# Kernel optimization log

Measured on AMD Instinct MI355X. Metric: run time of the kernel, lower is better.

## Reference

```python
import jax, jax.numpy as jnp
import numpy as np

EPS = 1e-5
NUM_CRYSTALS = 64


def _bn(x2d, g, b):
    # torch BatchNorm1d in training mode: biased batch stats, affine
    m = x2d.mean(0)
    v = x2d.var(0)
    return g * (x2d - m) * jax.lax.rsqrt(v + EPS) + b


def _improved_conv(x, e, idx, p):
    (fcW, fcb, g1, b1, g2, b2, eW, eb, ge, be, W3, b3, g3, b3b) = p
    N, M = idx.shape
    A = x.shape[1]
    Bf = e.shape[2]
    xn = x[idx]  # (N, M, A) gathered neighbor atom features
    tot = jnp.concatenate([jnp.broadcast_to(x[:, None, :], (N, M, A)), xn, e], axis=2)  # (N,M,2A+B)
    # 2-body gated message
    h = jnp.einsum('nmf,of->nmo', tot, fcW) + fcb
    h = _bn(h.reshape(-1, 2 * A), g1, b1).reshape(N, M, 2 * A)
    two_body = jnp.sum(jax.nn.sigmoid(h[..., :A]) * jax.nn.softplus(h[..., A:]), axis=1)
    # explicit edge update
    he = jnp.einsum('nmf,of->nmo', tot, eW) + eb
    he = _bn(he.reshape(-1, 2 * Bf), ge, be).reshape(N, M, 2 * Bf)
    e_out = e + jax.nn.sigmoid(he[..., :Bf]) * jax.nn.softplus(he[..., Bf:])
    # 3-body: split W3 by concat blocks [x_i, x_j, x_l, e_ij, e_il] so the
    # (N,M,M,3A+2B) concat is never materialized; only (N,M,M,2A) is formed.
    Wa, Wj, Wl, Wij, Wil = jnp.split(W3, [A, 2 * A, 3 * A, 3 * A + Bf], axis=1)
    h3 = ((x @ Wa.T)[:, None, None, :]
          + (xn @ Wj.T)[:, :, None, :]
          + (xn @ Wl.T)[:, None, :, :]
          + (e @ Wij.T)[:, :, None, :]
          + (e @ Wil.T)[:, None, :, :]
          + b3)  # (N, M, M, 2A)
    h3 = _bn(h3.reshape(-1, 2 * A), g3, b3b).reshape(N, M, M, 2 * A)
    three_body = jnp.sum(jax.nn.sigmoid(h3[..., :A]) * jax.nn.softplus(h3[..., A:]), axis=(1, 2))
    total = _bn(two_body + three_body, g2, b2)
    return jax.nn.softplus(x + total), e_out


def setup_inputs() -> dict:
    key = jax.random.key(0)
    ks = jax.random.split(key, 12)
    N, M, OF, A, BF, H, NC = 2000, 12, 92, 64, 41, 128, 3
    f = lambda k, s: jax.random.normal(k, s, dtype=jnp.float32) * 0.05
    z = lambda s: jnp.zeros(s, jnp.float32)
    o = lambda s: jnp.ones(s, jnp.float32)
    return {
        'atom_fea': jax.random.normal(ks[0], (N, OF), dtype=jnp.float32),
        'nbr_fea': jax.random.normal(ks[1], (N, M, BF), dtype=jnp.float32),
        'nbr_fea_idx': jax.random.randint(ks[2], (N, M), 0, N),
        'site_seg': jnp.sort(jax.random.randint(ks[3], (N,), 0, NUM_CRYSTALS)),
        'emb_W': f(ks[4], (A, OF)), 'emb_b': z((A,)),
        'fcW': f(ks[5], (NC, 2 * A, 2 * A + BF)), 'fcb': z((NC, 2 * A)),
        'bn1_g': o((NC, 2 * A)), 'bn1_b': z((NC, 2 * A)),
        'bn2_g': o((NC, A)), 'bn2_b': z((NC, A)),
        'eW': f(ks[6], (NC, 2 * BF, 2 * A + BF)), 'eb': z((NC, 2 * BF)),
        'bne_g': o((NC, 2 * BF)), 'bne_b': z((NC, 2 * BF)),
        'W3': f(ks[7], (NC, 2 * A, 3 * A + 2 * BF)), 'b3': z((NC, 2 * A)),
        'bn3_g': o((NC, 2 * A)), 'bn3_b': z((NC, 2 * A)),
        'fc1W': f(ks[8], (H, A)), 'fc1b': z((H,)),
        'outW': f(ks[9], (1, H)), 'outb': z((1,)),
    }


def reference(atom_fea, nbr_fea, nbr_fea_idx, site_seg, emb_W, emb_b,
              fcW, fcb, bn1_g, bn1_b, bn2_g, bn2_b, eW, eb, bne_g, bne_b,
              W3, b3, bn3_g, bn3_b, fc1W, fc1b, outW, outb):
    x = atom_fea @ emb_W.T + emb_b  # embedding1 (orbital=False)
    e = nbr_fea
    n_conv = fcW.shape[0]
    for i in range(n_conv):  # small fixed layer loop
        p = (fcW[i], fcb[i], bn1_g[i], bn1_b[i], bn2_g[i], bn2_b[i],
             eW[i], eb[i], bne_g[i], bne_b[i], W3[i], b3[i], bn3_g[i], bn3_b[i])
        x, e = _improved_conv(x, e, nbr_fea_idx, p)
    x = jax.nn.softplus(jax.nn.softplus(x) @ fc1W.T + fc1b)  # conv_to_fc1
    # per-crystal mean pooling over site segments
    N = x.shape[0]
    sums = jax.ops.segment_sum(x, site_seg, num_segments=NUM_CRYSTALS)
    counts = jax.ops.segment_sum(jnp.ones((N, 1), x.dtype), site_seg, num_segments=NUM_CRYSTALS)
    pooled = sums / jnp.maximum(counts, 1.0)
    return pooled @ outW.T + outb  # (NUM_CRYSTALS, 1)
```

## Files before the change

### kernel.cpp

```cpp
#include <hip/hip_runtime.h>
#include <hip/hip_bf16.h>

#define N_ATOM 2000
#define MNBR   12
#define OFEA   92
#define AF     64
#define BFEA   41
#define K1     169
#define O1     128
#define OE     82
#define NM     24000
#define NCONV  3
#define HID    128
#define NCRY   64
#define EPS_BN 1e-5f

#define LDA_T  192
#define LDH    512
#define LDSW   88
#define LDE    48

typedef __bf16 bf16x8 __attribute__((ext_vector_type(8)));
typedef float  f32x4  __attribute__((ext_vector_type(4)));

__device__ __forceinline__ float sigmoidf_(float x){
    return __builtin_amdgcn_rcpf(1.f + __expf(-x));
}
__device__ __forceinline__ float softplusf_(float x){
    return fmaxf(x,0.f) + __logf(1.f + __expf(-fabsf(x)));
}
__device__ __forceinline__ uint4 pack_bf16_8(const float* v){
    __hip_bfloat16 o[8];
    #pragma unroll
    for (int j=0;j<8;j++) o[j] = __float2bfloat16(v[j]);
    return *(const uint4*)o;
}

__global__ __launch_bounds__(256, 3)
void gemm_fused(const float* __restrict__ X,
                const float* __restrict__ E48,
                const int*   __restrict__ idx,
                const __hip_bfloat16* __restrict__ W,
                const float* __restrict__ bias,
                float* __restrict__ REST,
                float* __restrict__ STL,
                float* __restrict__ SPA,
                float* __restrict__ SQA)
{
    __shared__ unsigned short As[128][LDSW];
    __shared__ unsigned short Ws[128][LDSW];
    __shared__ float cs1[128];
    __shared__ float cs2[128];
    __shared__ float spa[12][128];

    const int tid  = threadIdx.x;
    const int row0 = blockIdx.x * 128;
    const int col0 = blockIdx.y * 128;
    const int w    = tid >> 6;
    const int l    = tid & 63;
    const int wm   = w >> 1, wn = w & 1;
    const int lrow = l & 15;
    const int quad = l >> 4;

    if (tid < 128){ cs1[tid] = 0.f; cs2[tid] = 0.f; }
    for (int ii = tid; ii < 12*128; ii += 256) spa[ii>>7][ii&127] = 0.f;

    f32x4 acc[4][4];
    #pragma unroll
    for (int i=0;i<4;i++)
        #pragma unroll
        for (int j=0;j<4;j++) acc[i][j] = (f32x4){0.f,0.f,0.f,0.f};

    #pragma unroll
    for (int it = 0; it < 3; ++it){
        const int k0 = it * 64;
        if (it) __syncthreads();
        #pragma unroll
        for (int j = 0; j < 4; ++j){
            int e  = tid + j*256;
            int r  = e >> 3;
            int kk = (e & 7) << 3;
            int grow = row0 + r;
            float v[8];
            #pragma unroll
            for (int q2=0;q2<8;q2++) v[q2] = 0.f;
            if (grow < NM){
                if (it == 2){
                    if (kk < LDE){
                        const float* s = E48 + (size_t)grow*LDE + kk;
                        float4 a0 = *(const float4*)s;
                        float4 a1 = *(const float4*)(s+4);
                        v[0]=a0.x; v[1]=a0.y; v[2]=a0.z; v[3]=a0.w;
                        v[4]=a1.x; v[5]=a1.y; v[6]=a1.z; v[7]=a1.w;
                    }
                } else {
                    const float* s = (it == 0)
                        ? X + (size_t)((unsigned)grow/12u)*AF + kk
                        : X + (size_t)idx[grow]*AF + kk;
                    float4 a0 = *(const float4*)s;
                    float4 a1 = *(const float4*)(s+4);
                    v[0]=a0.x; v[1]=a0.y; v[2]=a0.z; v[3]=a0.w;
                    v[4]=a1.x; v[5]=a1.y; v[6]=a1.z; v[7]=a1.w;
                }
            }
            *(uint4*)(&As[r][kk]) = pack_bf16_8(v);
            uint4 vw = *(const uint4*)(W + (size_t)(col0 + r)*LDA_T + k0 + kk);
            *(uint4*)(&Ws[r][kk]) = vw;
        }
        __syncthreads();
        #pragma unroll
        for (int ks = 0; ks < 2; ++ks){
            int koff = ks*32 + quad*8;
            bf16x8 a_[4], b_[4];
            #pragma unroll
            for (int mi=0;mi<4;mi++)
                a_[mi] = *(const bf16x8*)(&As[wm*64 + mi*16 + lrow][koff]);
            #pragma unroll
            for (int ni=0;ni<4;ni++)
                b_[ni] = *(const bf16x8*)(&Ws[wn*64 + ni*16 + lrow][koff]);
            #pragma unroll
            for (int mi=0;mi<4;mi++)
                #pragma unroll
                for (int ni=0;ni<4;ni++)
                    acc[mi][ni] = __builtin_amdgcn_mfma_f32_16x16x32_bf16(
                        a_[mi], b_[ni], acc[mi][ni], 0, 0, 0);
        }
    }

    const bool isPQ = (col0 >= 256);
    const int atomBase = (unsigned)row0 / 12u;
    int rbase_[4], n0_[4], sp_[4];
    #pragma unroll
    for (int mi=0;mi<4;mi++){
        rbase_[mi] = row0 + wm*64 + mi*16 + quad*4;
        int n0 = (int)((unsigned)rbase_[mi] / 12u);
        n0_[mi] = n0;
        sp_[mi] = 12 - (rbase_[mi] - n0*12);
    }

    #pragma unroll
    for (int ni=0;ni<4;ni++){
        const int cl  = wn*64 + ni*16 + lrow;
        const int col = col0 + cl;
        const float bv = bias[col];
        float s1 = 0.f, s2 = 0.f;
        #pragma unroll
        for (int mi=0;mi<4;mi++){
            const int rbase = rbase_[mi];
            float run0 = 0.f, run1 = 0.f;
            #pragma unroll
            for (int reg=0;reg<4;reg++){
                int grow = rbase + reg;
                if (grow < NM){
                    float vv = acc[mi][ni][reg] + bv;
                    if (col0 != 128 || col < 210)
                        REST[(size_t)grow*LDH + col] = vv;
                    s1 += vv; s2 += vv*vv;
                    if (isPQ){
                        if (reg < sp_[mi]) run0 += vv; else run1 += vv;
                    }
                }
            }
            if (isPQ){
                if (run0 != 0.f) atomicAdd(&spa[n0_[mi]     - atomBase][cl], run0);
                if (run1 != 0.f) atomicAdd(&spa[n0_[mi] + 1 - atomBase][cl], run1);
            }
        }
        if (isPQ){
            atomicAdd(&cs2[cl], s2);
        } else {
            atomicAdd(&cs1[cl], s1);
            atomicAdd(&cs2[cl], s2);
        }
    }
    __syncthreads();
    if (!isPQ){
        if (tid < 128){
            atomicAdd(&STL[col0 + tid],       cs1[tid]);
            atomicAdd(&STL[256 + col0 + tid], cs2[tid]);
        }
    } else {
        if (tid < 128)
            atomicAdd(&STL[(col0 == 256 ? 896 : 1024) + tid], cs2[tid]);
        float* SPQd = (col0 == 256) ? SPA : SQA;
        for (int ii = tid; ii < 12*128; ii += 256){
            int ai = ii >> 7, c2 = ii & 127;
            int na = atomBase + ai;
            float val = spa[ai][c2];
            if (val != 0.f && na < N_ATOM)
                atomicAdd(&SPQd[(size_t)na*128 + c2], val);
        }
    }
}

__global__ __launch_bounds__(256)
void bn3_pre(const float* __restrict__ SPA, const float* __restrict__ SQA,
             float* __restrict__ STL)
{
    const int c    = threadIdx.x & 127;
    const int half = threadIdx.x >> 7;
    float s1 = 0.f, sx = 0.f;
    for (int n = blockIdx.x*2 + half; n < N_ATOM; n += 64){
        float p = SPA[(size_t)n*128 + c];
        float q = SQA[(size_t)n*128 + c];
        s1 += p + q;
        sx += p * q;
    }
    atomicAdd(&STL[512 + c], 12.f*s1);
    atomicAdd(&STL[640 + c], 2.f*sx);
}

__global__ __launch_bounds__(256)
void emb_k(const float* __restrict__ A, const float* __restrict__ Wm,
           const float* __restrict__ b, float* __restrict__ X)
{
    __shared__ float Ws[64][93];
    __shared__ float As[16][93];
    const int t = threadIdx.x;
    const int n0 = blockIdx.x * 16;
    for (int i = t; i < 64*OFEA; i += 256){
        int c = i / OFEA, k = i % OFEA;
        Ws[c][k] = Wm[i];
    }
    for (int i = t; i < 16*OFEA; i += 256){
        int r = i / OFEA, k = i % OFEA;
        As[r][k] = A[(size_t)(n0 + r)*OFEA + k];
    }
    __syncthreads();
    const int r  = t >> 4;
    const int c0 = (t & 15) * 4;
    float a0=0.f, a1=0.f, a2=0.f, a3=0.f;
    for (int k = 0; k < OFEA; ++k){
        float av = As[r][k];
        a0 += av * Ws[c0+0][k];
        a1 += av * Ws[c0+1][k];
        a2 += av * Ws[c0+2][k];
        a3 += av * Ws[c0+3][k];
    }
    size_t o = (size_t)(n0 + r)*AF + c0;
    X[o+0] = a0 + b[c0+0];
    X[o+1] = a1 + b[c0+1];
    X[o+2] = a2 + b[c0+2];
    X[o+3] = a3 + b[c0+3];
}

__global__ __launch_bounds__(256)
void head_k(const float* __restrict__ X, const float* __restrict__ Wm,
            const float* __restrict__ b, float* __restrict__ Z)
{
    __shared__ float Ws[128][65];
    __shared__ float Xs[16][65];
    const int t = threadIdx.x;
    const int n0 = blockIdx.x * 16;
    for (int i = t; i < 128*AF; i += 256){
        int c = i >> 6, k = i & 63;
        Ws[c][k] = Wm[i];
    }
    for (int i = t; i < 16*AF; i += 256){
        int r = i >> 6, k = i & 63;
        Xs[r][k] = softplusf_(X[(size_t)(n0 + r)*AF + k]);
    }
    __syncthreads();
    const int r  = t >> 4;
    const int c0 = (t & 15) * 8;
    float acc[8];
    #pragma unroll
    for (int j=0;j<8;j++) acc[j] = 0.f;
    for (int k = 0; k < AF; ++k){
        float xv = Xs[r][k];
        #pragma unroll
        for (int j=0;j<8;j++)
            acc[j] += xv * Ws[c0+j][k];
    }
    size_t o = (size_t)(n0 + r)*HID + c0;
    #pragma unroll
    for (int j=0;j<8;j++)
        Z[o+j] = softplusf_(acc[j] + b[c0+j]);
}

__global__ void pack_all(const float* __restrict__ fcW, const float* __restrict__ eW,
                         const float* __restrict__ W3, const float* __restrict__ fcb,
                         const float* __restrict__ eb, const float* __restrict__ b3,
                         __hip_bfloat16* __restrict__ WALL, float* __restrict__ BIAS)
{
    int i = blockIdx.x*blockDim.x + threadIdx.x;
    const int nW = NCONV*512*LDA_T;
    if (i < nW){
        int ll = i/(512*LDA_T), rem = i%(512*LDA_T);
        int c = rem/LDA_T, k = rem%LDA_T;
        float v = 0.f;
        if (c < O1){
            if (k < K1) v = fcW[((size_t)ll*O1 + c)*K1 + k];
        } else if (c < O1+OE){
            if (k < K1) v = eW[((size_t)ll*OE + (c-O1))*K1 + k];
        } else if (c >= 256 && c < 384){
            int o = c - 256;
            const float* W3l = W3 + (size_t)ll*O1*274;
            if (k < AF)                        v = 0.5f * W3l[(size_t)o*274 + k];
            else if (k < 2*AF)                 v = W3l[(size_t)o*274 + k];
            else if (k < K1)                   v = W3l[(size_t)o*274 + 192 + (k-128)];
        } else if (c >= 384){
            int o = c - 384;
            const float* W3l = W3 + (size_t)ll*O1*274;
            if (k < AF)                        v = 0.5f * W3l[(size_t)o*274 + k];
            else if (k < 2*AF)                 v = W3l[(size_t)o*274 + k + AF];
            else if (k < K1)                   v = W3l[(size_t)o*274 + 233 + (k-128)];
        }
        WALL[i] = __float2bfloat16(v);
    } else if (i < nW + NCONV*512){
        int m = i - nW;
        int ll = m/512, c = m%512;
        float v = 0.f;
        if (c < O1)         v = fcb[ll*O1 + c];
        else if (c < O1+OE) v = eb[ll*OE + (c-O1)];
        else if (c >= 256)  v = 0.5f * b3[ll*O1 + ((c-256)&127)];
        BIAS[m] = v;
    }
}

__global__ void e_init(const float* __restrict__ nbr, float* __restrict__ E48)
{
    int i = blockIdx.x*blockDim.x + threadIdx.x;
    if (i >= NM*LDE) return;
    int r = i / LDE, k = i % LDE;
    E48[i] = (k < BFEA) ? nbr[(size_t)r*BFEA + k] : 0.f;
}

__global__ __launch_bounds__(256)
void consumer_k(const float* __restrict__ REST, const float* __restrict__ STL,
                float* __restrict__ TB, float* __restrict__ E48,
                const float* __restrict__ g1, const float* __restrict__ b1,
                const float* __restrict__ ge, const float* __restrict__ be,
                const float* __restrict__ g3, const float* __restrict__ b3b)
{
    __shared__ float red[256];
    __shared__ float scA[210], shA[210], sc3v[128], sh3v[128];
    const int n = blockIdx.x;
    const int t = threadIdx.x;
    const int a = t & 63;
    const int g = t >> 6;

    if (t < 210){
        float mean = STL[t]*(1.f/NM);
        float var  = fmaxf(STL[256+t]*(1.f/NM) - mean*mean, 0.f);
        float gg = (t < O1) ? g1[t] : ge[t-O1];
        float bb = (t < O1) ? b1[t] : be[t-O1];
        float sc = gg * rsqrtf(var + EPS_BN);
        scA[t] = sc; shA[t] = bb - sc*mean;
    }
    if (t < 128){
        float inv  = 1.f/((float)NM*MNBR);
        float mean = STL[512+t]*inv;
        float ex2  = (STL[640+t] + 12.f*(STL[896+t] + STL[1024+t]))*inv;
        float var  = fmaxf(ex2 - mean*mean, 0.f);
        float sc = g3[t] * rsqrtf(var + EPS_BN);
        sc3v[t] = sc; sh3v[t] = b3b[t] - sc*mean;
    }
    __syncthreads();

    const float* base = REST + (size_t)n*MNBR*LDH;
    const float s3lo = sc3v[a],  s3hi = sc3v[64+a];
    const float t3lo = sh3v[a],  t3hi = sh3v[64+a];

    float Ea[MNBR], Fb[MNBR];
    #pragma unroll
    for (int m=0;m<MNBR;m++){
        const float* row = base + (size_t)m*LDH;
        Ea[m] = __expf(-(s3lo*row[384+a]));
        Fb[m] = __expf( (s3hi*row[448+a]));
    }
    const float sha = scA[a],    tha = shA[a];
    const float shb = scA[64+a], thb = shA[64+a];
    float acc = 0.f;
    #pragma unroll
    for (int j=0;j<3;j++){
        const float* row = base + (size_t)(g*3+j)*LDH;
        acc += sigmoidf_(sha*row[a]+tha) * softplusf_(shb*row[64+a]+thb);
        float ua = s3lo*row[256+a] + t3lo;
        float ub = s3hi*row[320+a] + t3hi;
        float Em = __expf(-ua);
        float Fm = __expf(ub);
        #pragma unroll
        for (int l2=0;l2<MNBR;l2++){
            float s = __builtin_amdgcn_rcpf(1.f + Em*Ea[l2]);
            float p = __logf(1.f + Fm*Fb[l2]);
            acc += s*p;
        }
    }
    red[t] = acc;
    __syncthreads();
    if (t < 64)
        TB[(size_t)n*AF + t] = red[t] + red[64+t] + red[128+t] + red[192+t];
    for (int idx = t; idx < MNBR*BFEA; idx += 256){
        int m = idx / BFEA, b = idx % BFEA;
        const float* row = base + (size_t)m*LDH;
        float u = scA[O1+b]*row[O1+b]   + shA[O1+b];
        float v = scA[169+b]*row[169+b] + shA[169+b];
        E48[((size_t)n*MNBR + m)*LDE + b] += sigmoidf_(u) * softplusf_(v);
    }
}

__global__ __launch_bounds__(64)
void tb_stats_k(const float* __restrict__ TB,
                float* __restrict__ S1, float* __restrict__ S2)
{
    int t = threadIdx.x;
    float s1 = 0.f, s2 = 0.f;
    for (int r = blockIdx.x; r < N_ATOM; r += gridDim.x){
        float v = TB[(size_t)r*AF + t];
        s1 += v; s2 += v*v;
    }
    atomicAdd(&S1[t], s1);
    atomicAdd(&S2[t], s2);
}

__global__ void x_update_k(float* __restrict__ X, const float* __restrict__ TB,
                           const float* __restrict__ S12, const float* __restrict__ S22,
                           const float* __restrict__ g2, const float* __restrict__ b2,
                           int total)
{
    int i = blockIdx.x*blockDim.x + threadIdx.x;
    if (i >= total) return;
    int a = i & (AF-1);
    float mean = S12[a]*(1.f/N_ATOM);
    float var  = fmaxf(S22[a]*(1.f/N_ATOM) - mean*mean, 0.f);
    float sc = g2[a]*rsqrtf(var + EPS_BN);
    X[i] = softplusf_(X[i] + sc*TB[i] + (b2[a] - sc*mean));
}

__global__ __launch_bounds__(128)
void pool_out_k(const float* __restrict__ Z, const int* __restrict__ seg,
                const float* __restrict__ outW, const float* __restrict__ outb,
                float* __restrict__ out)
{
    __shared__ float red[128];
    const int c = blockIdx.x;
    const int h = threadIdx.x;
    int l0, l1;
    {
        int l=0, r=N_ATOM;
        while (l<r){ int m=(l+r)>>1; if (seg[m] < c) l=m+1; else r=m; }
        l0 = l;
        l=l0; r=N_ATOM;
        while (l<r){ int m=(l+r)>>1; if (seg[m] < c+1) l=m+1; else r=m; }
        l1 = l;
    }
    float s = 0.f;
    for (int n = l0; n < l1; ++n) s += Z[(size_t)n*HID + h];
    float cnt = fmaxf((float)(l1-l0), 1.f);
    red[h] = (s/cnt) * outW[h];
    __syncthreads();
    for (int off=64; off>0; off>>=1){
        if (h < off) red[h] += red[h+off];
        __syncthreads();
    }
    if (h == 0) out[c] = red[0] + outb[0];
}

extern "C" void kernel_launch(void* const* d_in, const int* in_sizes, int n_in,
                              void* d_out, int out_size, void* d_ws, size_t ws_size,
                              hipStream_t stream)
{
    const float* atom_fea = (const float*)d_in[0];
    const float* nbr_fea  = (const float*)d_in[1];
    const int*   nbr_idx  = (const int*)d_in[2];
    const int*   site_seg = (const int*)d_in[3];
    const float* emb_W = (const float*)d_in[4];
    const float* emb_b = (const float*)d_in[5];
    const float* fcW   = (const float*)d_in[6];
    const float* fcb   = (const float*)d_in[7];
    const float* bn1_g = (const float*)d_in[8];
    const float* bn1_b = (const float*)d_in[9];
    const float* bn2_g = (const float*)d_in[10];
    const float* bn2_b = (const float*)d_in[11];
    const float* eW    = (const float*)d_in[12];
    const float* eb    = (const float*)d_in[13];
    const float* bne_g = (const float*)d_in[14];
    const float* bne_b = (const float*)d_in[15];
    const float* W3    = (const float*)d_in[16];
    const float* b3    = (const float*)d_in[17];
    const float* bn3_g = (const float*)d_in[18];
    const float* bn3_b = (const float*)d_in[19];
    const float* fc1W  = (const float*)d_in[20];
    const float* fc1b  = (const float*)d_in[21];
    const float* outW  = (const float*)d_in[22];
    const float* outb  = (const float*)d_in[23];

    float* ws   = (float*)d_ws;
    float* X    = ws;
    float* E48  = ws + 128000;
    float* REST = ws + 1280000;
    float* TB   = ws + 13568000;
    float* Z    = ws + 13696000;
    float* ST   = ws + 13952000;
    float* SCu  = ws + 13958144;
    float* SPQ  = ws + 13959168;
    __hip_bfloat16* WALL = (__hip_bfloat16*)(ws + 15495168);
    float* BIAS = ws + 15642624;
    (void)SCu;

    {
        int tot = NCONV*512*LDA_T + NCONV*512;
        pack_all<<<(tot+255)/256, 256, 0, stream>>>(fcW, eW, W3, fcb, eb, b3, WALL, BIAS);
    }
    hipMemsetAsync(ST, 0, (size_t)(6144 + 1024 + 1536000) * sizeof(float), stream);
    emb_k<<<N_ATOM/16, 256, 0, stream>>>(atom_fea, emb_W, emb_b, X);
    e_init<<<(NM*LDE+255)/256, 256, 0, stream>>>(nbr_fea, E48);

    for (int i = 0; i < NCONV; i++){
        float* STL = ST + i*2048;
        float* SPA = SPQ + (size_t)i*512000;
        float* SQA = SPA + 256000;

        {
            dim3 g((NM+127)/128, 4);
            gemm_fused<<<g, 256, 0, stream>>>(X, E48, nbr_idx,
                                              WALL + (size_t)i*512*LDA_T,
                                              BIAS + i*512, REST, STL, SPA, SQA);
        }
        bn3_pre<<<32, 256, 0, stream>>>(SPA, SQA, STL);
        consumer_k<<<N_ATOM, 256, 0, stream>>>(REST, STL, TB, E48,
                                               bn1_g + i*O1, bn1_b + i*O1,
                                               bne_g + i*OE, bne_b + i*OE,
                                               bn3_g + i*O1, bn3_b + i*O1);
        tb_stats_k<<<128, 64, 0, stream>>>(TB, STL+768, STL+832);
        x_update_k<<<(N_ATOM*AF+255)/256, 256, 0, stream>>>(X, TB, STL+768, STL+832,
                                                            bn2_g + i*AF, bn2_b + i*AF,
                                                            N_ATOM*AF);
    }

    head_k<<<N_ATOM/16, 256, 0, stream>>>(X, fc1W, fc1b, Z);
    pool_out_k<<<NCRY, 128, 0, stream>>>(Z, site_seg, outW, outb, (float*)d_out);
}
```

Before: 355.8 us.

## Keep bf16 shadow copies of activations and fuse prologue and BN2 update kernels

```diff
diff --git a/kernel.cpp b/kernel.cpp
--- a/kernel.cpp
+++ b/kernel.cpp
@@ -29,16 +29,10 @@
 __device__ __forceinline__ float softplusf_(float x){
     return fmaxf(x,0.f) + __logf(1.f + __expf(-fabsf(x)));
 }
-__device__ __forceinline__ uint4 pack_bf16_8(const float* v){
-    __hip_bfloat16 o[8];
-    #pragma unroll
-    for (int j=0;j<8;j++) o[j] = __float2bfloat16(v[j]);
-    return *(const uint4*)o;
-}
 
 __global__ __launch_bounds__(256, 3)
-void gemm_fused(const float* __restrict__ X,
-                const float* __restrict__ E48,
+void gemm_fused(const unsigned short* __restrict__ Xb,
+                const unsigned short* __restrict__ E48b,
                 const int*   __restrict__ idx,
                 const __hip_bfloat16* __restrict__ W,
                 const float* __restrict__ bias,
@@ -77,35 +71,25 @@
         if (it) __syncthreads();
         #pragma unroll
         for (int j = 0; j < 4; ++j){
-            int e  = tid + j*256;
-            int r  = e >> 3;
-            int kk = (e & 7) << 3;
+            int e   = tid + j*256;
+            int r   = e >> 3;
+            int kk8 = (e & 7);
             int grow = row0 + r;
-            float v[8];
-            #pragma unroll
-            for (int q2=0;q2<8;q2++) v[q2] = 0.f;
+            uint4 va = make_uint4(0,0,0,0);
             if (grow < NM){
                 if (it == 2){
-                    if (kk < LDE){
-                        const float* s = E48 + (size_t)grow*LDE + kk;
-                        float4 a0 = *(const float4*)s;
-                        float4 a1 = *(const float4*)(s+4);
-                        v[0]=a0.x; v[1]=a0.y; v[2]=a0.z; v[3]=a0.w;
-                        v[4]=a1.x; v[5]=a1.y; v[6]=a1.z; v[7]=a1.w;
-                    }
+                    if (kk8 < 6)
+                        va = *(const uint4*)(E48b + (size_t)grow*LDE + kk8*8);
                 } else {
-                    const float* s = (it == 0)
-                        ? X + (size_t)((unsigned)grow/12u)*AF + kk
-                        : X + (size_t)idx[grow]*AF + kk;
-                    float4 a0 = *(const float4*)s;
-                    float4 a1 = *(const float4*)(s+4);
-                    v[0]=a0.x; v[1]=a0.y; v[2]=a0.z; v[3]=a0.w;
-                    v[4]=a1.x; v[5]=a1.y; v[6]=a1.z; v[7]=a1.w;
+                    const unsigned short* s = (it == 0)
+                        ? Xb + (size_t)((unsigned)grow/12u)*AF + kk8*8
+                        : Xb + (size_t)idx[grow]*AF + kk8*8;
+                    va = *(const uint4*)s;
                 }
             }
-            *(uint4*)(&As[r][kk]) = pack_bf16_8(v);
-            uint4 vw = *(const uint4*)(W + (size_t)(col0 + r)*LDA_T + k0 + kk);
-            *(uint4*)(&Ws[r][kk]) = vw;
+            *(uint4*)(&As[r][kk8*8]) = va;
+            uint4 vw = *(const uint4*)(W + (size_t)(col0 + r)*LDA_T + k0 + kk8*8);
+            *(uint4*)(&Ws[r][kk8*8]) = vw;
         }
         __syncthreads();
         #pragma unroll
@@ -200,7 +184,7 @@
     const int c    = threadIdx.x & 127;
     const int half = threadIdx.x >> 7;
     float s1 = 0.f, sx = 0.f;
-    for (int n = blockIdx.x*2 + half; n < N_ATOM; n += 64){
+    for (int n = blockIdx.x*2 + half; n < N_ATOM; n += 250){
         float p = SPA[(size_t)n*128 + c];
         float q = SQA[(size_t)n*128 + c];
         s1 += p + q;
@@ -212,7 +196,8 @@
 
 __global__ __launch_bounds__(256)
 void emb_k(const float* __restrict__ A, const float* __restrict__ Wm,
-           const float* __restrict__ b, float* __restrict__ X)
+           const float* __restrict__ b, float* __restrict__ X,
+           __hip_bfloat16* __restrict__ Xb)
 {
     __shared__ float Ws[64][93];
     __shared__ float As[16][93];
@@ -238,10 +223,11 @@
         a3 += av * Ws[c0+3][k];
     }
     size_t o = (size_t)(n0 + r)*AF + c0;
-    X[o+0] = a0 + b[c0+0];
-    X[o+1] = a1 + b[c0+1];
-    X[o+2] = a2 + b[c0+2];
-    X[o+3] = a3 + b[c0+3];
+    float v0 = a0 + b[c0+0], v1 = a1 + b[c0+1];
+    float v2 = a2 + b[c0+2], v3 = a3 + b[c0+3];
+    X[o+0] = v0; X[o+1] = v1; X[o+2] = v2; X[o+3] = v3;
+    Xb[o+0] = __float2bfloat16(v0); Xb[o+1] = __float2bfloat16(v1);
+    Xb[o+2] = __float2bfloat16(v2); Xb[o+3] = __float2bfloat16(v3);
 }
 
 __global__ __launch_bounds__(256)
@@ -278,13 +264,18 @@
         Z[o+j] = softplusf_(acc[j] + b[c0+j]);
 }
 
-__global__ void pack_all(const float* __restrict__ fcW, const float* __restrict__ eW,
-                         const float* __restrict__ W3, const float* __restrict__ fcb,
-                         const float* __restrict__ eb, const float* __restrict__ b3,
-                         __hip_bfloat16* __restrict__ WALL, float* __restrict__ BIAS)
+__global__ void prologue_k(const float* __restrict__ fcW, const float* __restrict__ eW,
+                           const float* __restrict__ W3, const float* __restrict__ fcb,
+                           const float* __restrict__ eb, const float* __restrict__ b3,
+                           const float* __restrict__ nbr,
+                           __hip_bfloat16* __restrict__ WALL, float* __restrict__ BIAS,
+                           float* __restrict__ E48, __hip_bfloat16* __restrict__ E48b,
+                           float* __restrict__ ZR)
 {
     int i = blockIdx.x*blockDim.x + threadIdx.x;
     const int nW = NCONV*512*LDA_T;
+    const int nB = NCONV*512;
+    const int nE = NM*LDE;
     if (i < nW){
         int ll = i/(512*LDA_T), rem = i%(512*LDA_T);
         int c = rem/LDA_T, k = rem%LDA_T;
@@ -307,7 +298,7 @@
             else if (k < K1)                   v = W3l[(size_t)o*274 + 233 + (k-128)];
         }
         WALL[i] = __float2bfloat16(v);
-    } else if (i < nW + NCONV*512){
+    } else if (i < nW + nB){
         int m = i - nW;
         int ll = m/512, c = m%512;
         float v = 0.f;
@@ -315,20 +306,22 @@
         else if (c < O1+OE) v = eb[ll*OE + (c-O1)];
         else if (c >= 256)  v = 0.5f * b3[ll*O1 + ((c-256)&127)];
         BIAS[m] = v;
-    }
-}
-
-__global__ void e_init(const float* __restrict__ nbr, float* __restrict__ E48)
-{
-    int i = blockIdx.x*blockDim.x + threadIdx.x;
-    if (i >= NM*LDE) return;
-    int r = i / LDE, k = i % LDE;
-    E48[i] = (k < BFEA) ? nbr[(size_t)r*BFEA + k] : 0.f;
+    } else if (i < nW + nB + nE){
+        int j = i - (nW + nB);
+        int r = j / LDE, k = j % LDE;
+        float v = (k < BFEA) ? nbr[(size_t)r*BFEA + k] : 0.f;
+        E48[j]  = v;
+        E48b[j] = __float2bfloat16(v);
+    } else {
+        int j = i - (nW + nB + nE);
+        ZR[j] = 0.f;
+    }
 }
 
 __global__ __launch_bounds__(256)
 void consumer_k(const float* __restrict__ REST, const float* __restrict__ STL,
                 float* __restrict__ TB, float* __restrict__ E48,
+                __hip_bfloat16* __restrict__ E48b,
                 const float* __restrict__ g1, const float* __restrict__ b1,
                 const float* __restrict__ ge, const float* __restrict__ be,
                 const float* __restrict__ g3, const float* __restrict__ b3b)
@@ -396,36 +389,53 @@
         const float* row = base + (size_t)m*LDH;
         float u = scA[O1+b]*row[O1+b]   + shA[O1+b];
         float v = scA[169+b]*row[169+b] + shA[169+b];
-        E48[((size_t)n*MNBR + m)*LDE + b] += sigmoidf_(u) * softplusf_(v);
-    }
-}
-
-__global__ __launch_bounds__(64)
-void tb_stats_k(const float* __restrict__ TB,
-                float* __restrict__ S1, float* __restrict__ S2)
-{
-    int t = threadIdx.x;
+        size_t eo = ((size_t)n*MNBR + m)*LDE + b;
+        float nv = E48[eo] + sigmoidf_(u) * softplusf_(v);
+        E48[eo]  = nv;
+        E48b[eo] = __float2bfloat16(nv);
+    }
+}
+
+__global__ __launch_bounds__(256)
+void xupd_k(float* __restrict__ X, __hip_bfloat16* __restrict__ Xb,
+            const float* __restrict__ TB, float* __restrict__ STL,
+            const float* __restrict__ g2, const float* __restrict__ b2)
+{
+    __shared__ float r1[256], r2[256];
+    const int t = threadIdx.x;
+    const int a = t & 63, rg = t >> 6;
     float s1 = 0.f, s2 = 0.f;
-    for (int r = blockIdx.x; r < N_ATOM; r += gridDim.x){
-        float v = TB[(size_t)r*AF + t];
+    for (int r = blockIdx.x*4 + rg; r < N_ATOM; r += 256){
+        float v = TB[(size_t)r*AF + a];
         s1 += v; s2 += v*v;
     }
-    atomicAdd(&S1[t], s1);
-    atomicAdd(&S2[t], s2);
-}
-
-__global__ void x_update_k(float* __restrict__ X, const float* __restrict__ TB,
-                           const float* __restrict__ S12, const float* __restrict__ S22,
-                           const float* __restrict__ g2, const float* __restrict__ b2,
-                           int total)
-{
-    int i = blockIdx.x*blockDim.x + threadIdx.x;
-    if (i >= total) return;
-    int a = i & (AF-1);
-    float mean = S12[a]*(1.f/N_ATOM);
-    float var  = fmaxf(S22[a]*(1.f/N_ATOM) - mean*mean, 0.f);
+    r1[t] = s1; r2[t] = s2;
+    __syncthreads();
+    if (t < 64){
+        s1 = r1[t]+r1[64+t]+r1[128+t]+r1[192+t];
+        s2 = r2[t]+r2[64+t]+r2[128+t]+r2[192+t];
+        atomicAdd(&STL[768+t], s1);
+        atomicAdd(&STL[832+t], s2);
+    }
+    __syncthreads();
+    if (t == 0){
+        unsigned* cnt = (unsigned*)&STL[1200];
+        __hip_atomic_fetch_add(cnt, 1u, __ATOMIC_ACQ_REL, __HIP_MEMORY_SCOPE_AGENT);
+        while (__hip_atomic_load(cnt, __ATOMIC_ACQUIRE, __HIP_MEMORY_SCOPE_AGENT) < 64u)
+            __builtin_amdgcn_s_sleep(2);
+    }
+    __syncthreads();
+    float sA = __hip_atomic_load(&STL[768+a], __ATOMIC_RELAXED, __HIP_MEMORY_SCOPE_AGENT);
+    float sB = __hip_atomic_load(&STL[832+a], __ATOMIC_RELAXED, __HIP_MEMORY_SCOPE_AGENT);
+    float mean = sA*(1.f/N_ATOM);
+    float var  = fmaxf(sB*(1.f/N_ATOM) - mean*mean, 0.f);
     float sc = g2[a]*rsqrtf(var + EPS_BN);
-    X[i] = softplusf_(X[i] + sc*TB[i] + (b2[a] - sc*mean));
+    float sh = b2[a] - sc*mean;
+    for (int i = blockIdx.x*256 + t; i < N_ATOM*AF; i += 64*256){
+        float v = softplusf_(X[i] + sc*TB[i] + sh);
+        X[i]  = v;
+        Xb[i] = __float2bfloat16(v);
+    }
 }
 
 __global__ __launch_bounds__(128)
@@ -493,19 +503,18 @@
     float* TB   = ws + 13568000;
     float* Z    = ws + 13696000;
     float* ST   = ws + 13952000;
-    float* SCu  = ws + 13958144;
     float* SPQ  = ws + 13959168;
     __hip_bfloat16* WALL = (__hip_bfloat16*)(ws + 15495168);
     float* BIAS = ws + 15642624;
-    (void)SCu;
+    __hip_bfloat16* Xb   = (__hip_bfloat16*)(ws + 15644160);
+    __hip_bfloat16* E48b = (__hip_bfloat16*)(ws + 15708160);
 
     {
-        int tot = NCONV*512*LDA_T + NCONV*512;
-        pack_all<<<(tot+255)/256, 256, 0, stream>>>(fcW, eW, W3, fcb, eb, b3, WALL, BIAS);
-    }
-    hipMemsetAsync(ST, 0, (size_t)(6144 + 1024 + 1536000) * sizeof(float), stream);
-    emb_k<<<N_ATOM/16, 256, 0, stream>>>(atom_fea, emb_W, emb_b, X);
-    e_init<<<(NM*LDE+255)/256, 256, 0, stream>>>(nbr_fea, E48);
+        const int total = 294912 + 1536 + 1152000 + 1543168;
+        prologue_k<<<total/256, 256, 0, stream>>>(fcW, eW, W3, fcb, eb, b3, nbr_fea,
+                                                  WALL, BIAS, E48, E48b, ST);
+    }
+    emb_k<<<N_ATOM/16, 256, 0, stream>>>(atom_fea, emb_W, emb_b, X, Xb);
 
     for (int i = 0; i < NCONV; i++){
         float* STL = ST + i*2048;
@@ -514,19 +523,18 @@
 
         {
             dim3 g((NM+127)/128, 4);
-            gemm_fused<<<g, 256, 0, stream>>>(X, E48, nbr_idx,
+            gemm_fused<<<g, 256, 0, stream>>>((const unsigned short*)Xb,
+                                              (const unsigned short*)E48b, nbr_idx,
                                               WALL + (size_t)i*512*LDA_T,
                                               BIAS + i*512, REST, STL, SPA, SQA);
         }
-        bn3_pre<<<32, 256, 0, stream>>>(SPA, SQA, STL);
-        consumer_k<<<N_ATOM, 256, 0, stream>>>(REST, STL, TB, E48,
+        bn3_pre<<<125, 256, 0, stream>>>(SPA, SQA, STL);
+        consumer_k<<<N_ATOM, 256, 0, stream>>>(REST, STL, TB, E48, E48b,
                                                bn1_g + i*O1, bn1_b + i*O1,
                                                bne_g + i*OE, bne_b + i*OE,
                                                bn3_g + i*O1, bn3_b + i*O1);
-        tb_stats_k<<<128, 64, 0, stream>>>(TB, STL+768, STL+832);
-        x_update_k<<<(N_ATOM*AF+255)/256, 256, 0, stream>>>(X, TB, STL+768, STL+832,
-                                                            bn2_g + i*AF, bn2_b + i*AF,
-                                                            N_ATOM*AF);
+        xupd_k<<<64, 256, 0, stream>>>(X, Xb, TB, STL,
+                                       bn2_g + i*AF, bn2_b + i*AF);
     }
 
     head_k<<<N_ATOM/16, 256, 0, stream>>>(X, fc1W, fc1b, Z);
```

New measurement: 353.1 us (median of 2 runs). About the same (-0.8%).
